# Performance work log

Measured on AMD Instinct MI355X. Metric: run time of the kernel, lower is better.

## Reference

```python
import jax, jax.numpy as jnp
import numpy as np

TABLE_SIZE = 256
I16_MIN, I16_MAX = -32768.0, 32767.0
I8_MIN, I8_MAX = -128.0, 127.0
MAX_SOFTMAX_VALUE = 1.0
OUT_SCALE = MAX_SOFTMAX_VALUE * 2.0 / 255.0            # int8 output scale
EXP_OUT_SCALE = 2.0 / 65535.0                          # qint16 exp output scale
RECIP_OUT_SCALE = (1.0 / 0.1) * 2.0 / 65535.0          # qint16 reciprocal output scale
# (xmin, xmax, kind) in ascending x order; 'table' = 256-entry LUT, 'line' = linear fit
EXP_REGIONS = [(-40.0, -20.0, 'line'), (-20.0, -10.0, 'table'), (-10.0, 0.0, 'table'), (0.0, 1.0, 'line')]
RECIP_REGIONS = [(0.001, 0.1, 'line'), (0.1, 250.0, 'table'), (250.0, 500.0, 'table'), (500.0, 700.0, 'line')]


def _quant(y, out_scale, qmin, qmax):
    return jnp.clip(jnp.round(y / out_scale), qmin, qmax)


def _piecewise(x, func, regions, out_scale, qmin, qmax):
    """Piecewise quantized approximation of func: constant / line / 256-entry
    table regions, returning quantized (integer-valued float) outputs."""
    left_c = _quant(func(jnp.float32(regions[0][0])), out_scale, qmin, qmax)
    y = left_c * jnp.ones_like(x)
    for xmin, xmax, kind in regions:
        if kind == 'table':
            xs = jnp.linspace(xmin, xmax, TABLE_SIZE)
            tab = _quant(func(xs), out_scale, qmin, qmax)
            idx = jnp.clip(jnp.round((x - xmin) * ((TABLE_SIZE - 1) / (xmax - xmin))), 0, TABLE_SIZE - 1).astype(jnp.int32)
            y_r = tab[idx]
        else:
            y0 = func(jnp.float32(xmin))
            y1 = func(jnp.float32(xmax))
            y_r = _quant(y0 + (x - xmin) * ((y1 - y0) / (xmax - xmin)), out_scale, qmin, qmax)
        y = jnp.where(x >= xmin, y_r, y)
    right_c = _quant(func(jnp.float32(regions[-1][1])), out_scale, qmin, qmax)
    return jnp.where(x > regions[-1][1], right_c, y)


def setup_inputs() -> dict:
    key = jax.random.key(0)
    k1, _ = jax.random.split(key)
    data = jax.random.randint(k1, (32, 128, 80, 80), -128, 128, dtype=jnp.int32)  # int8 repr, zp=0
    data_scale = jnp.array([0.0625], dtype=jnp.float32)
    return {"data": data, "data_scale": data_scale}


def reference(data, data_scale):
    ds = data_scale[0]
    C = data.shape[1]
    shift = float(np.ceil(np.log2(C)))  # rescale_shift for the exp-sum
    # max-subtract in the integer domain, dequantize diff (zero_point = 0)
    qmax = jnp.max(data, axis=1, keepdims=True)
    xd = (data - qmax).astype(jnp.float32) * ds  # [B,C,H,W], in (-inf, 0]
    # quantized exp via piecewise tables -> qint16 with EXP_OUT_SCALE
    exp_q = _piecewise(xd, jnp.exp, EXP_REGIONS, EXP_OUT_SCALE, I16_MIN, I16_MAX)
    # sum over channels, right-shift back into int16 range
    sum_q = jnp.sum(exp_q, axis=1, keepdims=True)
    sum_sh = jnp.clip(jnp.round(sum_q * (2.0 ** -shift)), I16_MIN, I16_MAX)
    div_scale = EXP_OUT_SCALE * (2.0 ** shift)  # div_data_scale
    # quantized reciprocal of the (dequantized) shifted sum -> qint16
    recip_q = _piecewise(sum_sh * div_scale, lambda v: 1.0 / v, RECIP_REGIONS, RECIP_OUT_SCALE, I16_MIN, I16_MAX)
    # out = exp * recip, requantized to int8 with OUT_SCALE, then dequantized
    out_q = jnp.clip(jnp.round(exp_q * recip_q * (EXP_OUT_SCALE * RECIP_OUT_SCALE / OUT_SCALE)), I8_MIN, I8_MAX)
    return out_q * OUT_SCALE
```

## Files before the change

kernel.cpp:

```cpp
#include <hip/hip_runtime.h>
#include <cmath>

#define NB  32
#define NC  128
#define NHW 6400
#define PIX 64
#define TPB 256

typedef float vfloat4 __attribute__((ext_vector_type(4)));


__global__ __launch_bounds__(TPB) void qsoftmax_kernel(
    const int* __restrict__ data,
    const float* __restrict__ dscale,
    float* __restrict__ out) {
#pragma clang fp contract(off)
  __shared__ int   exp_tab[256];
  __shared__ float recip_tab[256];

  const int t   = threadIdx.x;
  const int l   = t & 63;
  const int w   = t >> 6;
  const int kq  = (l >> 2) & 15;
  const int qw  = (w << 2) | (l & 3);

  const int blk  = blockIdx.x;
  const int b    = blk / (NHW / PIX);
  const int hw0  = (blk % (NHW / PIX)) * PIX;
  const int base4 = b * NC * (NHW / 4) + (hw0 >> 2) + qw;

  const float ds = dscale[0];

  {
    const float EXP_SCALE_F = (float)(2.0 / 65535.0);
    float x = (float)(-t) * ds;
    float e;
    if (x >= 0.0f) {
      float y0 = expf(0.0f), y1 = expf(1.0f);
      e = rintf((y0 + x * ((y1 - y0) / 1.0f)) / EXP_SCALE_F);
    } else if (x >= -10.0f) {
      float delta = 10.0f / 255.0f;
      float idxf = rintf((x + 10.0f) * 25.5f);
      idxf = fminf(fmaxf(idxf, 0.0f), 255.0f);
      float xs = -10.0f + idxf * delta;
      e = rintf((float)exp((double)xs) / EXP_SCALE_F);
    } else {
      float delta = 10.0f / 255.0f;
      float idxf = rintf((x + 20.0f) * 25.5f);
      idxf = fminf(fmaxf(idxf, 0.0f), 255.0f);
      float xs = -20.0f + idxf * delta;
      e = rintf((float)exp((double)xs) / EXP_SCALE_F);
    }
    e = fminf(fmaxf(e, -32768.0f), 32767.0f);
    exp_tab[t] = (int)e;

    const float RECIP_SCALE_F = (float)((1.0 / 0.1) * 2.0 / 65535.0);
    float deltar = (250.0f - 0.1f) / 255.0f;
    float xs = 0.1f + (float)t * deltar;
    float r = rintf((1.0f / xs) / RECIP_SCALE_F);
    r = fminf(fmaxf(r, -32768.0f), 32767.0f);
    recip_tab[t] = r;
  }
  __syncthreads();

  const int4* g4 = (const int4*)data;
  int pd[8];
  int4 m = make_int4(-128, -128, -128, -128);
#pragma unroll
  for (int i = 0; i < 8; ++i) {
    int4 v = g4[base4 + (16 * i + kq) * (NHW / 4)];
    m.x = max(m.x, v.x); m.y = max(m.y, v.y);
    m.z = max(m.z, v.z); m.w = max(m.w, v.w);
    pd[i] = (v.x & 255) | ((v.y & 255) << 8) | ((v.z & 255) << 16) |
            (int)((unsigned)(v.w & 255) << 24);
  }

#pragma unroll
  for (int xm = 4; xm <= 32; xm <<= 1) {
    m.x = max(m.x, __shfl_xor(m.x, xm, 64));
    m.y = max(m.y, __shfl_xor(m.y, xm, 64));
    m.z = max(m.z, __shfl_xor(m.z, xm, 64));
    m.w = max(m.w, __shfl_xor(m.w, xm, 64));
  }

  int pe[16];
  int4 s = make_int4(0, 0, 0, 0);
#pragma unroll
  for (int i = 0; i < 8; ++i) {
    int pdv = pd[i];
    int c0 = (pdv << 24) >> 24;
    int c1 = (pdv << 16) >> 24;
    int c2 = (pdv << 8) >> 24;
    int c3 = pdv >> 24;
    int e0 = exp_tab[m.x - c0];
    int e1 = exp_tab[m.y - c1];
    int e2 = exp_tab[m.z - c2];
    int e3 = exp_tab[m.w - c3];
    s.x += e0; s.y += e1; s.z += e2; s.w += e3;
    pe[2 * i]     = e0 | (e1 << 16);
    pe[2 * i + 1] = e2 | (e3 << 16);
  }

#pragma unroll
  for (int xm = 4; xm <= 32; xm <<= 1) {
    s.x += __shfl_xor(s.x, xm, 64);
    s.y += __shfl_xor(s.y, xm, 64);
    s.z += __shfl_xor(s.z, xm, 64);
    s.w += __shfl_xor(s.w, xm, 64);
  }

  const float DIV_SCALE_F = (float)((2.0 / 65535.0) * 128.0);
  const float RIDX_K_F    = (float)(255.0 / (250.0 - 0.1));
  float rq[4];
  {
    int tv[4] = {s.x, s.y, s.z, s.w};
#pragma unroll
    for (int j = 0; j < 4; ++j) {
      float ss = rintf((float)tv[j] * 0.0078125f);
      ss = fminf(fmaxf(ss, -32768.0f), 32767.0f);
      float v = ss * DIV_SCALE_F;
      float idxf = rintf((v - 0.1f) * RIDX_K_F);
      idxf = fminf(fmaxf(idxf, 0.0f), 255.0f);
      rq[j] = recip_tab[(int)idxf];
    }
  }

  const float K_F = (float)((2.0 / 65535.0) * ((1.0 / 0.1) * 2.0 / 65535.0) / (2.0 / 255.0));
  const float OUT_SCALE_F = (float)(2.0 / 255.0);
  vfloat4* o4 = (vfloat4*)out;
#pragma unroll
  for (int i = 0; i < 8; ++i) {
    int pa = pe[2 * i], pb = pe[2 * i + 1];
    float e0 = (float)(pa & 0xFFFF);
    float e1 = (float)(pa >> 16);
    float e2 = (float)(pb & 0xFFFF);
    float e3 = (float)(pb >> 16);
    vfloat4 o;
    o.x = fminf(fmaxf(rintf((e0 * rq[0]) * K_F), -128.0f), 127.0f) * OUT_SCALE_F;
    o.y = fminf(fmaxf(rintf((e1 * rq[1]) * K_F), -128.0f), 127.0f) * OUT_SCALE_F;
    o.z = fminf(fmaxf(rintf((e2 * rq[2]) * K_F), -128.0f), 127.0f) * OUT_SCALE_F;
    o.w = fminf(fmaxf(rintf((e3 * rq[3]) * K_F), -128.0f), 127.0f) * OUT_SCALE_F;
    __builtin_nontemporal_store(o, &o4[base4 + (16 * i + kq) * (NHW / 4)]);
  }
}

extern "C" void kernel_launch(void* const* d_in, const int* in_sizes, int n_in,
                              void* d_out, int out_size, void* d_ws, size_t ws_size,
                              hipStream_t stream) {
  const int* data     = (const int*)d_in[0];
  const float* dscale = (const float*)d_in[1];
  float* out          = (float*)d_out;
  (void)in_sizes; (void)n_in; (void)d_ws; (void)ws_size; (void)out_size;

  dim3 grid(NB * (NHW / PIX));
  qsoftmax_kernel<<<grid, TPB, 0, stream>>>(data, dscale, out);
}
```

Before: 199.1 us.

## Precompute LUTs in separate kernel and use single-wave blocks with 32 channels per thread

Moves construction of the exp and reciprocal lookup tables into a small prior kernel that writes them to workspace, so each softmax block only copies them into LDS instead of evaluating exp/double math per block. Blocks shrink from 256 to 64 threads (one wave), and each thread now handles 32 channel rows instead of 8, which cuts the shuffle reduction steps and removes cross-wave coordination. The cost is much higher register use (pd[32], pe[64]) and less memory-level parallelism per block, plus an extra kernel launch.

```diff
diff --git a/kernel.cpp b/kernel.cpp
--- a/kernel.cpp
+++ b/kernel.cpp
@@ -4,71 +4,78 @@
 #define NB  32
 #define NC  128
 #define NHW 6400
-#define PIX 64
-#define TPB 256
+#define TPB 64
 
 typedef float vfloat4 __attribute__((ext_vector_type(4)));
 
+__global__ __launch_bounds__(64) void lut_build_kernel(
+    int* __restrict__ exp_ws, float* __restrict__ rec_ws,
+    const float* __restrict__ dscale) {
+#pragma clang fp contract(off)
+  const int t = blockIdx.x * 64 + threadIdx.x;
+  const float ds = dscale[0];
 
-__global__ __launch_bounds__(TPB) void qsoftmax_kernel(
+  const float EXP_SCALE_F = (float)(2.0 / 65535.0);
+  float x = (float)(-t) * ds;
+  float e;
+  if (x >= 0.0f) {
+    float y0 = expf(0.0f), y1 = expf(1.0f);
+    e = rintf((y0 + x * ((y1 - y0) / 1.0f)) / EXP_SCALE_F);
+  } else if (x >= -10.0f) {
+    float delta = 10.0f / 255.0f;
+    float idxf = rintf((x + 10.0f) * 25.5f);
+    idxf = fminf(fmaxf(idxf, 0.0f), 255.0f);
+    float xs = -10.0f + idxf * delta;
+    e = rintf((float)exp((double)xs) / EXP_SCALE_F);
+  } else {
+    float delta = 10.0f / 255.0f;
+    float idxf = rintf((x + 20.0f) * 25.5f);
+    idxf = fminf(fmaxf(idxf, 0.0f), 255.0f);
+    float xs = -20.0f + idxf * delta;
+    e = rintf((float)exp((double)xs) / EXP_SCALE_F);
+  }
+  e = fminf(fmaxf(e, -32768.0f), 32767.0f);
+  exp_ws[t] = (int)e;
+
+  const float RECIP_SCALE_F = (float)((1.0 / 0.1) * 2.0 / 65535.0);
+  float deltar = (250.0f - 0.1f) / 255.0f;
+  float xs = 0.1f + (float)t * deltar;
+  float r = rintf((1.0f / xs) / RECIP_SCALE_F);
+  r = fminf(fmaxf(r, -32768.0f), 32767.0f);
+  rec_ws[t] = r;
+}
+
+__global__ __launch_bounds__(TPB, 4) void qsoftmax_kernel(
     const int* __restrict__ data,
-    const float* __restrict__ dscale,
+    const int* __restrict__ exp_ws,
+    const float* __restrict__ rec_ws,
     float* __restrict__ out) {
 #pragma clang fp contract(off)
   __shared__ int   exp_tab[256];
   __shared__ float recip_tab[256];
 
-  const int t   = threadIdx.x;
-  const int l   = t & 63;
-  const int w   = t >> 6;
-  const int kq  = (l >> 2) & 15;
-  const int qw  = (w << 2) | (l & 3);
+  const int t  = threadIdx.x;
+  const int cg = t >> 4;
+  const int p4 = t & 15;
 
   const int blk  = blockIdx.x;
-  const int b    = blk / (NHW / PIX);
-  const int hw0  = (blk % (NHW / PIX)) * PIX;
-  const int base4 = b * NC * (NHW / 4) + (hw0 >> 2) + qw;
-
-  const float ds = dscale[0];
+  const int b    = blk / (NHW / 64);
+  const int hw0  = (blk % (NHW / 64)) * 64;
+  const int base4 = b * NC * (NHW / 4) + (hw0 >> 2) + p4;
 
   {
-    const float EXP_SCALE_F = (float)(2.0 / 65535.0);
-    float x = (float)(-t) * ds;
-    float e;
-    if (x >= 0.0f) {
-      float y0 = expf(0.0f), y1 = expf(1.0f);
-      e = rintf((y0 + x * ((y1 - y0) / 1.0f)) / EXP_SCALE_F);
-    } else if (x >= -10.0f) {
-      float delta = 10.0f / 255.0f;
-      float idxf = rintf((x + 10.0f) * 25.5f);
-      idxf = fminf(fmaxf(idxf, 0.0f), 255.0f);
-      float xs = -10.0f + idxf * delta;
-      e = rintf((float)exp((double)xs) / EXP_SCALE_F);
-    } else {
-      float delta = 10.0f / 255.0f;
-      float idxf = rintf((x + 20.0f) * 25.5f);
-      idxf = fminf(fmaxf(idxf, 0.0f), 255.0f);
-      float xs = -20.0f + idxf * delta;
-      e = rintf((float)exp((double)xs) / EXP_SCALE_F);
-    }
-    e = fminf(fmaxf(e, -32768.0f), 32767.0f);
-    exp_tab[t] = (int)e;
-
-    const float RECIP_SCALE_F = (float)((1.0 / 0.1) * 2.0 / 65535.0);
-    float deltar = (250.0f - 0.1f) / 255.0f;
-    float xs = 0.1f + (float)t * deltar;
-    float r = rintf((1.0f / xs) / RECIP_SCALE_F);
-    r = fminf(fmaxf(r, -32768.0f), 32767.0f);
-    recip_tab[t] = r;
+    int4   ev = ((const int4*)exp_ws)[t];
+    float4 rv = ((const float4*)rec_ws)[t];
+    ((int4*)exp_tab)[t]     = ev;
+    ((float4*)recip_tab)[t] = rv;
   }
-  __syncthreads();
 
   const int4* g4 = (const int4*)data;
-  int pd[8];
+  int pd[32];
   int4 m = make_int4(-128, -128, -128, -128);
 #pragma unroll
-  for (int i = 0; i < 8; ++i) {
-    int4 v = g4[base4 + (16 * i + kq) * (NHW / 4)];
+  for (int i = 0; i < 32; ++i) {
+    int4 v = g4[base4 + (4 * i + cg) * (NHW / 4)];
     m.x = max(m.x, v.x); m.y = max(m.y, v.y);
     m.z = max(m.z, v.z); m.w = max(m.w, v.w);
     pd[i] = (v.x & 255) | ((v.y & 255) << 8) | ((v.z & 255) << 16) |
@@ -76,17 +83,19 @@
   }
 
 #pragma unroll
-  for (int xm = 4; xm <= 32; xm <<= 1) {
+  for (int xm = 16; xm <= 32; xm <<= 1) {
     m.x = max(m.x, __shfl_xor(m.x, xm, 64));
     m.y = max(m.y, __shfl_xor(m.y, xm, 64));
     m.z = max(m.z, __shfl_xor(m.z, xm, 64));
     m.w = max(m.w, __shfl_xor(m.w, xm, 64));
   }
 
-  int pe[16];
+  __syncthreads();
+
+  int pe[64];
   int4 s = make_int4(0, 0, 0, 0);
 #pragma unroll
-  for (int i = 0; i < 8; ++i) {
+  for (int i = 0; i < 32; ++i) {
     int pdv = pd[i];
     int c0 = (pdv << 24) >> 24;
     int c1 = (pdv << 16) >> 24;
@@ -102,7 +111,7 @@
   }
 
 #pragma unroll
-  for (int xm = 4; xm <= 32; xm <<= 1) {
+  for (int xm = 16; xm <= 32; xm <<= 1) {
     s.x += __shfl_xor(s.x, xm, 64);
     s.y += __shfl_xor(s.y, xm, 64);
     s.z += __shfl_xor(s.z, xm, 64);
@@ -129,7 +138,7 @@
   const float OUT_SCALE_F = (float)(2.0 / 255.0);
   vfloat4* o4 = (vfloat4*)out;
 #pragma unroll
-  for (int i = 0; i < 8; ++i) {
+  for (int i = 0; i < 32; ++i) {
     int pa = pe[2 * i], pb = pe[2 * i + 1];
     float e0 = (float)(pa & 0xFFFF);
     float e1 = (float)(pa >> 16);
@@ -140,7 +149,7 @@
     o.y = fminf(fmaxf(rintf((e1 * rq[1]) * K_F), -128.0f), 127.0f) * OUT_SCALE_F;
     o.z = fminf(fmaxf(rintf((e2 * rq[2]) * K_F), -128.0f), 127.0f) * OUT_SCALE_F;
     o.w = fminf(fmaxf(rintf((e3 * rq[3]) * K_F), -128.0f), 127.0f) * OUT_SCALE_F;
-    __builtin_nontemporal_store(o, &o4[base4 + (16 * i + kq) * (NHW / 4)]);
+    __builtin_nontemporal_store(o, &o4[base4 + (4 * i + cg) * (NHW / 4)]);
   }
 }
 
@@ -150,8 +159,12 @@
   const int* data     = (const int*)d_in[0];
   const float* dscale = (const float*)d_in[1];
   float* out          = (float*)d_out;
-  (void)in_sizes; (void)n_in; (void)d_ws; (void)ws_size; (void)out_size;
+  (void)in_sizes; (void)n_in; (void)out_size; (void)ws_size;
 
-  dim3 grid(NB * (NHW / PIX));
-  qsoftmax_kernel<<<grid, TPB, 0, stream>>>(data, dscale, out);
+  int*   exp_ws = (int*)d_ws;
+  float* rec_ws = (float*)((char*)d_ws + 1024);
+
+  lut_build_kernel<<<dim3(4), dim3(64), 0, stream>>>(exp_ws, rec_ws, dscale);
+  qsoftmax_kernel<<<dim3(NB * (NHW / 64)), dim3(TPB), 0, stream>>>(
+      data, exp_ws, rec_ws, out);
 }
```

Result: slower. 278.7 us (+40.0%).
